# Kernel tuning notes

Measured on AMD Instinct MI355X. Metric: run time of the kernel, lower is better.

The kernel has to match this reference:

```python
import jax, jax.numpy as jnp
from jax import lax
import numpy as np

V, T, K, R, H, EN, L = 10000, 100, 50, 300, 200, 800, 3
B = 128
TRAIN_SIZE = 100000
DELTA = 0.005


def setup_inputs():
    key = jax.random.key(0)
    ks = jax.random.split(key, 16)
    s = 0.02
    return {
        "bows": jax.random.uniform(ks[0], (B, V), jnp.float32) * 10.0 + 1e-3,
        "times": jax.random.randint(ks[1], (B,), 0, T),
        "rnn_inp": jax.random.uniform(ks[2], (T, V), jnp.float32),
        "rho_W": jax.random.normal(ks[3], (V, R), jnp.float32) * s,
        "mu_q_alpha": jax.random.normal(ks[4], (K, T, R), jnp.float32),
        "logsigma_q_alpha": jax.random.normal(ks[5], (K, T, R), jnp.float32) * 0.1 - 2.0,
        "qtheta_W1": jax.random.normal(ks[6], (EN, V + K), jnp.float32) * s,
        "qtheta_b1": jnp.zeros((EN,), jnp.float32),
        "qtheta_W2": jax.random.normal(ks[7], (EN, EN), jnp.float32) * s,
        "qtheta_b2": jnp.zeros((EN,), jnp.float32),
        "mu_theta_W": jax.random.normal(ks[8], (K, EN), jnp.float32) * s,
        "mu_theta_b": jnp.zeros((K,), jnp.float32),
        "ls_theta_W": jax.random.normal(ks[9], (K, EN), jnp.float32) * s,
        "ls_theta_b": jnp.zeros((K,), jnp.float32),
        "eta_map_W": jax.random.normal(ks[10], (H, V), jnp.float32) * s,
        "eta_map_b": jnp.zeros((H,), jnp.float32),
        "lstm_Wih": jax.random.normal(ks[11], (L, 4 * H, H), jnp.float32) * s,
        "lstm_Whh": jax.random.normal(ks[12], (L, 4 * H, H), jnp.float32) * s,
        "lstm_bih": jnp.zeros((L, 4 * H), jnp.float32),
        "lstm_bhh": jnp.zeros((L, 4 * H), jnp.float32),
        "mu_eta_W": jax.random.normal(ks[13], (K, H + K), jnp.float32) * s,
        "mu_eta_b": jnp.zeros((K,), jnp.float32),
        "ls_eta_W": jax.random.normal(ks[14], (K, H + K), jnp.float32) * s,
        "ls_eta_b": jnp.zeros((K,), jnp.float32),
    }


def _kl(q_mu, q_ls, p_mu, p_ls):
    # KL(N(q_mu, exp(q_ls)) || N(p_mu, exp(p_ls))), logsigma == log-variance as in torch code
    return 0.5 * jnp.sum((jnp.exp(q_ls) + (q_mu - p_mu) ** 2) / (jnp.exp(p_ls) + 1e-6) - 1.0 + p_ls - q_ls, axis=-1)


def _lstm(x, Wih, Whh, bih, bhh):
    # x: [T, H]; L stacked LSTM layers (batch of 1 squeezed), torch gate order i,f,g,o
    for l in range(Wih.shape[0]):
        Wi, Wh, bi, bh = Wih[l], Whh[l], bih[l], bhh[l]
        Hd = Wh.shape[1]

        def step(carry, xt, Wi=Wi, Wh=Wh, bi=bi, bh=bh):
            h, c = carry
            g = Wi @ xt + Wh @ h + bi + bh
            i, f, gg, o = jnp.split(g, 4)
            c = jax.nn.sigmoid(f) * c + jax.nn.sigmoid(i) * jnp.tanh(gg)
            h = jax.nn.sigmoid(o) * jnp.tanh(c)
            return (h, c), h

        z = jnp.zeros((Hd,), x.dtype)
        _, x = lax.scan(step, (z, z), x)
    return x


def _forward(bows, rnn_inp, rho_W, mu_q_alpha, logsigma_q_alpha, qtheta_W1, qtheta_b1, qtheta_W2, qtheta_b2, mu_theta_W, mu_theta_b, ls_theta_W, ls_theta_b, eta_map_W, eta_map_b, lstm_Wih, lstm_Whh, lstm_bih, lstm_bhh, mu_eta_W, mu_eta_b, ls_eta_W, ls_eta_b, times):
    log_delta = jnp.log(jnp.float32(DELTA))
    # --- eta: LSTM over word-freq sequence, then sequential mu/logsigma/KL per t ---
    out = _lstm(rnn_inp @ eta_map_W.T + eta_map_b, lstm_Wih, lstm_Whh, lstm_bih, lstm_bhh)  # [T,H]
    p_ls_seq = jnp.concatenate([jnp.zeros((1,), jnp.float32), jnp.full((T - 1,), log_delta, jnp.float32)])

    def eta_step(eta_prev, xs):
        o_t, p_ls = xs
        x = jnp.concatenate([o_t, eta_prev])
        mu = mu_eta_W @ x + mu_eta_b
        ls = ls_eta_W @ x + ls_eta_b
        kl = _kl(mu, ls, eta_prev, jnp.full_like(mu, p_ls))
        return mu, (mu, kl)  # eval-mode reparameterize -> eta_t = mu

    _, (etas, kls) = lax.scan(eta_step, jnp.zeros((K,), jnp.float32), (out, p_ls_seq))
    kl_eta = kls.sum()
    # --- theta encoder ---
    nb = bows / bows.sum(1, keepdims=True)
    eta_td = etas[times]  # [B,K]
    h = jax.nn.relu(jnp.concatenate([nb, eta_td], axis=1) @ qtheta_W1.T + qtheta_b1)
    h = jax.nn.relu(h @ qtheta_W2.T + qtheta_b2)
    mu_t = h @ mu_theta_W.T + mu_theta_b
    ls_t = h @ ls_theta_W.T + ls_theta_b
    theta = jax.nn.softmax(mu_t, axis=-1)  # z = mu (eval-mode reparam)
    coeff = jnp.float32(TRAIN_SIZE / bows.shape[0])
    kl_theta = _kl(mu_t, ls_t, eta_td, jnp.zeros_like(mu_t)).sum() * coeff
    # --- alpha: with eval-mode reparam, alphas == mu, so KL is fully vectorized ---
    muT = jnp.transpose(mu_q_alpha, (1, 0, 2))  # [T,K,R]
    lsT = jnp.transpose(logsigma_q_alpha, (1, 0, 2))
    alphas = muT
    p_mu = jnp.concatenate([jnp.zeros((1, K, R), muT.dtype), alphas[:-1]], axis=0)
    p_ls = jnp.concatenate([jnp.zeros((1, K, R), muT.dtype), jnp.full((T - 1, K, R), log_delta, muT.dtype)], axis=0)
    kl_alpha = _kl(muT, lsT, p_mu, p_ls).sum()
    # --- beta and NLL ---
    logit = alphas.reshape(T * K, R) @ rho_W.T  # [T*K, V]
    beta = jax.nn.softmax(logit, axis=-1).reshape(T, K, V)
    beta_d = beta[times]  # [B,K,V]
    loglik = jnp.log(jnp.einsum('bk,bkv->bv', theta, beta_d) + 1e-12)
    nll = (-(loglik * bows).sum(-1)).sum() * coeff
    loss = nll + kl_eta + kl_theta + kl_alpha
    return loss, nll, kl_eta, kl_theta, kl_alpha


def reference(bows, times, rnn_inp, rho_W, mu_q_alpha, logsigma_q_alpha, qtheta_W1, qtheta_b1, qtheta_W2, qtheta_b2, mu_theta_W, mu_theta_b, ls_theta_W, ls_theta_b, eta_map_W, eta_map_b, lstm_Wih, lstm_Whh, lstm_bih, lstm_bhh, mu_eta_W, mu_eta_b, ls_eta_W, ls_eta_b):
    return _forward(bows, rnn_inp, rho_W, mu_q_alpha, logsigma_q_alpha, qtheta_W1, qtheta_b1, qtheta_W2, qtheta_b2, mu_theta_W, mu_theta_b, ls_theta_W, ls_theta_b, eta_map_W, eta_map_b, lstm_Wih, lstm_Whh, lstm_bih, lstm_bhh, mu_eta_W, mu_eta_b, ls_eta_W, ls_eta_b, times)
```

## Files before the change

kernel.cpp:

```cpp
#include <hip/hip_runtime.h>


typedef unsigned int u32;
typedef unsigned short u16;
typedef _Float16 f16;
typedef f16 f16x2 __attribute__((ext_vector_type(2)));
typedef short bf16x8 __attribute__((ext_vector_type(8)));
typedef float f32x4 __attribute__((ext_vector_type(4)));
typedef u32 u32x4 __attribute__((ext_vector_type(4)));

#define LOG_DELTA (-5.2983174f)
#define COEFF 781.25f

#if defined(__has_builtin)
#if __has_builtin(__builtin_amdgcn_sdot4)
#define HAVE_SDOT4 1
#endif
#endif

__device__ __forceinline__ float bf2f(u16 a) { return __uint_as_float(((u32)a) << 16); }
__device__ __forceinline__ u16 f2bf(float f) {
  u32 u = __float_as_uint(f);
  u32 r = (u + 0x7fffu + ((u >> 16) & 1u)) >> 16;
  return (u16)r;
}
__device__ __forceinline__ int dot4i8(u32 a, u32 b, int c) {
#ifdef HAVE_SDOT4
  return __builtin_amdgcn_sdot4(a, b, c, false);
#else
  int s = c;
  s += ((int)(a << 24) >> 24) * ((int)(b << 24) >> 24);
  s += ((int)(a << 16) >> 24) * ((int)(b << 16) >> 24);
  s += ((int)(a << 8) >> 24) * ((int)(b << 8) >> 24);
  s += ((int)a >> 24) * ((int)b >> 24);
  return s;
#endif
}
__device__ __forceinline__ float sigm(float x) { return 1.f / (1.f + __expf(-x)); }
__device__ __forceinline__ float ftanh(float x) { float t = __expf(2.f * x); return (t - 1.f) / (t + 1.f); }
__device__ __forceinline__ u16 f2h(float x) { return __builtin_bit_cast(u16, (f16)x); }
__device__ __forceinline__ float h2f(u16 x) { return (float)__builtin_bit_cast(f16, x); }
__device__ __forceinline__ void async_load16(const u16* g, u16* l) {
  __builtin_amdgcn_global_load_lds((const __attribute__((address_space(1))) u32*)g,
                                   (__attribute__((address_space(3))) u32*)l, 16, 0, 0);
}

__device__ __forceinline__ void gbar(u32* bar, int idx, u32 target) {
  __syncthreads();
  __threadfence();
  if (threadIdx.x == 0) {
    atomicAdd(&bar[idx], 1u);
    while (atomicAdd(&bar[idx], 0u) < target) __builtin_amdgcn_s_sleep(8);
  }
  __threadfence();
  __syncthreads();
}


__global__ __launch_bounds__(256) void k_init(
    const float* __restrict__ bih, const float* __restrict__ bhh, float* __restrict__ bsum,
    const float* __restrict__ muthb, const float* __restrict__ lsthb, float* __restrict__ mul,
    const float* __restrict__ muq, const float* __restrict__ lsq, float* __restrict__ alphapart,
    float* __restrict__ accum, u32* __restrict__ bar) {
  const int bx = blockIdx.x, tid = threadIdx.x;
  if (bx < 10) {
    int i = bx * 256 + tid;
    if (i < 2400) bsum[i] = bih[i] + bhh[i];
    return;
  }
  if (bx == 10) {
    if (tid < 8) accum[tid] = 0.f;
    else if (tid < 16) bar[tid - 8] = 0u;
    return;
  }
  if (bx < 523) {
    __shared__ float red[256];
    float s = 0.f;
    for (int i = (bx - 11) * 256 + tid; i < 1500000; i += 512 * 256) {
      int r = i % 300;
      int tk = i / 300;
      int k = tk % 50;
      int t = tk / 50;
      size_t idx = (size_t)k * 30000 + (size_t)t * 300 + r;
      float mu = muq[idx], ls = lsq[idx];
      float pm = 0.f, pls = 0.f;
      if (t > 0) { pm = muq[idx - 300]; pls = LOG_DELTA; }
      float d = mu - pm;
      s += 0.5f * ((__expf(ls) + d * d) / (__expf(pls) + 1e-6f) - 1.f + pls - ls);
    }
    red[tid] = s; __syncthreads();
    for (int o = 128; o > 0; o >>= 1) { if (tid < o) red[tid] += red[tid + o]; __syncthreads(); }
    if (tid == 0) alphapart[bx - 11] = red[0];
    return;
  }
  {
    int i = (bx - 523) * 256 + tid;
    if (i < 12800) { int c = i % 100; mul[i] = (c < 50) ? muthb[c] : lsthb[c - 50]; }
  }
}


__global__ __launch_bounds__(256) void k_nbquant(
    const float* __restrict__ bows, float* __restrict__ nb,
    const float* __restrict__ Whh, u32* __restrict__ whq, float* __restrict__ rowscale) {
  const int tid = threadIdx.x;
  if (blockIdx.x < 128) {
    __shared__ float red[256];
    const int b = blockIdx.x;
    float s = 0.f;
    for (int v = tid; v < 10000; v += 256) s += bows[b * 10000 + v];
    red[tid] = s; __syncthreads();
    for (int o = 128; o > 0; o >>= 1) { if (tid < o) red[tid] += red[tid + o]; __syncthreads(); }
    const float inv = 1.f / red[0];
    for (int v = tid; v < 10000; v += 256) nb[b * 10000 + v] = bows[b * 10000 + v] * inv;
    return;
  }
  __shared__ float wrow[4][200];
  const int wave = tid >> 6, lane = tid & 63;
  const int gr = (blockIdx.x - 128) * 4 + wave;
  const float* src = Whh + (size_t)gr * 200;
  float m = 0.f;
  for (int c = lane; c < 200; c += 64) { float v = src[c]; wrow[wave][c] = v; m = fmaxf(m, fabsf(v)); }
  for (int o = 32; o > 0; o >>= 1) m = fmaxf(m, __shfl_down(m, o));
  m = __shfl(m, 0);
  const float qs = (m > 0.f) ? 127.f / m : 0.f;
  const int l = gr / 800, rr = gr - l * 800;
  if (lane < 52) {
    u32 d = 0;
    if (lane < 50) {
#pragma unroll
      for (int b = 0; b < 4; ++b) {
        int q = __float2int_rn(wrow[wave][lane * 4 + b] * qs);
        q = max(-127, min(127, q));
        d |= ((u32)(q & 0xff)) << (8 * b);
      }
    }
    whq[l * 41600 + rr * 52 + lane] = d;
  }
  if (lane == 0) rowscale[gr] = (m > 0.f) ? m / 127.f : 0.f;
}


__global__ __launch_bounds__(256) void k_prepAB(const float* __restrict__ muq,
                                                const float* __restrict__ rho,
                                                u16* __restrict__ Abf, u16* __restrict__ Bbf) {
  if (blockIdx.x < 6400) {
    int idx = blockIdx.x * 256 + threadIdx.x;
    if (idx >= 5120 * 320) return;
    int r = idx % 320, m = idx / 320;
    float v = 0.f;
    if (r < 300 && m < 5000) { int t = m / 50, k = m - t * 50; v = muq[k * 30000 + t * 300 + r]; }
    Abf[idx] = f2bf(v);
    return;
  }
  int idx = (blockIdx.x - 6400) * 256 + threadIdx.x;
  if (idx >= 10112 * 320) return;
  int r = idx % 320, n = idx / 320;
  float v = (r < 300 && n < 10000) ? rho[n * 300 + r] : 0.f;
  Bbf[idx] = f2bf(v);
}


#define ST 64
#define SBK 32

template<int AMODE, int BMODE, int EPI>
__global__ __launch_bounds__(256) void gemm64(
    const float* __restrict__ A, const float* __restrict__ Bm, const float* __restrict__ Bm2,
    const float* __restrict__ bias, float* __restrict__ C,
    int M, int N, int Kd, int lda, int ldb,
    const int* __restrict__ times, const float* __restrict__ etas)
{
  __shared__ __align__(16) float As[SBK][ST + 4];
  __shared__ __align__(16) float Bs[SBK][ST + 4];
  const int tid = threadIdx.x;
  const int tx = tid & 15, ty = tid >> 4;
  const int m_base = blockIdx.x * ST, n_base = blockIdx.y * ST;
  float acc[4][4] = {};
  const int nkt = (Kd + SBK - 1) / SBK;
  const int per = (nkt + gridDim.z - 1) / gridDim.z;
  const int kt0 = blockIdx.z * per;
  const int kt1 = min(nkt, kt0 + per);
  const int lkk = tid & 31;
  const int lrow = tid >> 5;
  for (int kt = kt0; kt < kt1; ++kt) {
    const int kg = kt * SBK + lkk;
#pragma unroll
    for (int i = 0; i < 8; ++i) {
      const int m = m_base + lrow + i * 8;
      float v = 0.f;
      if (m < M && kg < Kd) {
        if (AMODE == 0) v = A[(size_t)m * lda + kg];
        else {
          if (kg < 10000) v = A[(size_t)m * 10000 + kg];
          else v = etas[times[m] * 50 + (kg - 10000)];
        }
      }
      As[lkk][lrow + i * 8] = v;
    }
#pragma unroll
    for (int i = 0; i < 8; ++i) {
      const int n = n_base + lrow + i * 8;
      float v = 0.f;
      if (n < N && kg < Kd) {
        if (BMODE == 0) v = Bm[(size_t)n * ldb + kg];
        else v = (n < 50) ? Bm[(size_t)n * ldb + kg] : Bm2[(size_t)(n - 50) * ldb + kg];
      }
      Bs[lkk][lrow + i * 8] = v;
    }
    __syncthreads();
#pragma unroll
    for (int kk = 0; kk < SBK; ++kk) {
      const float4 a4 = *(const float4*)&As[kk][ty * 4];
      const float4 b4 = *(const float4*)&Bs[kk][tx * 4];
      const float av[4] = {a4.x, a4.y, a4.z, a4.w};
      const float bv[4] = {b4.x, b4.y, b4.z, b4.w};
#pragma unroll
      for (int i = 0; i < 4; ++i)
#pragma unroll
        for (int j = 0; j < 4; ++j) acc[i][j] += av[i] * bv[j];
    }
    __syncthreads();
  }
#pragma unroll
  for (int i = 0; i < 4; ++i) {
    const int m = m_base + ty * 4 + i;
    if (m >= M) continue;
#pragma unroll
    for (int j = 0; j < 4; ++j) {
      const int n = n_base + tx * 4 + j;
      if (n >= N) continue;
      float v = acc[i][j];
      if (EPI == 1) { C[(size_t)m * N + n] = v + bias[n]; }
      else if (EPI == 2) { v += bias[n]; C[(size_t)m * N + n] = v > 0.f ? v : 0.f; }
      else if (EPI == 5) { atomicAdd(&C[(size_t)m * N + n], v); }
      else { C[(size_t)m * N + n] = v; }
    }
  }
}


#define LT 128
#define LBK 32

template<int AMODE>
__global__ __launch_bounds__(256) void gemm128p(
    const float* __restrict__ A, const float* __restrict__ Bm,
    float* __restrict__ P,
    int M, int N, int Kd, int lda, int ldb,
    const int* __restrict__ times, const float* __restrict__ etas)
{
  __shared__ __align__(16) float As[LBK][LT + 4];
  __shared__ __align__(16) float Bs[LBK][LT + 4];
  const int tid = threadIdx.x;
  const int tx = tid & 15, ty = tid >> 4;
  const int m_base = blockIdx.x * LT, n_base = blockIdx.y * LT;
  const int nkt = (Kd + LBK - 1) / LBK;
  const int per = (nkt + gridDim.z - 1) / gridDim.z;
  const int kt0 = blockIdx.z * per;
  const int kt1 = min(nkt, kt0 + per);
  const int lkk = tid & 31;
  const int lrow = tid >> 5;
  float acc[8][8] = {};
  float pa[16], pb[16];
  {
    const int kg = kt0 * LBK + lkk;
#pragma unroll
    for (int i = 0; i < 16; ++i) {
      const int m = m_base + lrow + i * 8;
      float v = 0.f;
      if (m < M && kg < Kd) {
        if (AMODE == 0) v = A[(size_t)m * lda + kg];
        else v = (kg < 10000) ? A[(size_t)m * 10000 + kg] : etas[times[m] * 50 + (kg - 10000)];
      }
      pa[i] = v;
      const int n = n_base + lrow + i * 8;
      float w = 0.f;
      if (n < N && kg < Kd) w = Bm[(size_t)n * ldb + kg];
      pb[i] = w;
    }
  }
  for (int kt = kt0; kt < kt1; ++kt) {
#pragma unroll
    for (int i = 0; i < 16; ++i) {
      As[lkk][lrow + i * 8] = pa[i];
      Bs[lkk][lrow + i * 8] = pb[i];
    }
    __syncthreads();
    if (kt + 1 < kt1) {
      const int kg = (kt + 1) * LBK + lkk;
#pragma unroll
      for (int i = 0; i < 16; ++i) {
        const int m = m_base + lrow + i * 8;
        float v = 0.f;
        if (m < M && kg < Kd) {
          if (AMODE == 0) v = A[(size_t)m * lda + kg];
          else v = (kg < 10000) ? A[(size_t)m * 10000 + kg] : etas[times[m] * 50 + (kg - 10000)];
        }
        pa[i] = v;
        const int n = n_base + lrow + i * 8;
        float w = 0.f;
        if (n < N && kg < Kd) w = Bm[(size_t)n * ldb + kg];
        pb[i] = w;
      }
    }
#pragma unroll
    for (int kk = 0; kk < LBK; ++kk) {
      const float4* ap = (const float4*)&As[kk][ty * 8];
      const float4* bp = (const float4*)&Bs[kk][tx * 8];
      const float4 a0 = ap[0], a1 = ap[1];
      const float4 b0 = bp[0], b1 = bp[1];
      const float av[8] = {a0.x, a0.y, a0.z, a0.w, a1.x, a1.y, a1.z, a1.w};
      const float bv[8] = {b0.x, b0.y, b0.z, b0.w, b1.x, b1.y, b1.z, b1.w};
#pragma unroll
      for (int i = 0; i < 8; ++i)
#pragma unroll
        for (int j = 0; j < 8; ++j) acc[i][j] += av[i] * bv[j];
    }
    __syncthreads();
  }
  float* Cz = P + (size_t)blockIdx.z * M * N;
#pragma unroll
  for (int i = 0; i < 8; ++i) {
    const int m = m_base + ty * 8 + i;
    if (m >= M) continue;
#pragma unroll
    for (int j = 0; j < 8; ++j) {
      const int n = n_base + tx * 8 + j;
      if (n >= N) continue;
      Cz[(size_t)m * N + n] = acc[i][j];
    }
  }
}

template<int EPI>
__global__ __launch_bounds__(256) void k_reduceZ(const float* __restrict__ P,
                                                 const float* __restrict__ bias,
                                                 float* __restrict__ out,
                                                 int N, int total, int Z) {
  for (int i = blockIdx.x * 256 + threadIdx.x; i < total; i += gridDim.x * 256) {
    float s = bias[i % N];
    for (int z = 0; z < Z; ++z) s += P[(size_t)z * total + i];
    if (EPI == 2) s = s > 0.f ? s : 0.f;
    out[i] = s;
  }
}


__global__ __launch_bounds__(256) void gemm_mfma_bT(
    const u16* __restrict__ A, const u16* __restrict__ B, u16* __restrict__ C,
    int M, int N)
{
  __shared__ u16 As[128 * 32];
  __shared__ u16 Bs[128 * 32];
  const int tid = threadIdx.x;
  const int l = tid & 63, w = tid >> 6;
  const int wm = w & 1, wn = w >> 1;
  const int m0 = blockIdx.x * 128, n0 = blockIdx.y * 128;
  f32x4 acc[4][4] = {};
  const int arow = l >> 2;
  const int acol = (l & 3) * 8;
  for (int kt = 0; kt < 10; ++kt) {
    const int k0 = kt * 32;
#pragma unroll
    for (int c = 0; c < 2; ++c) {
      const int i = w + c * 4;
      async_load16(A + (size_t)(m0 + i * 16 + arow) * 320 + k0 + acol, As + i * 512);
      async_load16(B + (size_t)(n0 + i * 16 + arow) * 320 + k0 + acol, Bs + i * 512);
    }
    __syncthreads();
    bf16x8 af[4], bfr[4];
#pragma unroll
    for (int x = 0; x < 4; ++x) {
      af[x]  = *(const bf16x8*)&As[(wm * 64 + x * 16 + (l & 15)) * 32 + (l >> 4) * 8];
      bfr[x] = *(const bf16x8*)&Bs[(wn * 64 + x * 16 + (l & 15)) * 32 + (l >> 4) * 8];
    }
#pragma unroll
    for (int x = 0; x < 4; ++x)
#pragma unroll
      for (int y = 0; y < 4; ++y)
        acc[x][y] = __builtin_amdgcn_mfma_f32_16x16x32_bf16(af[x], bfr[y], acc[x][y], 0, 0, 0);
    __syncthreads();
  }
  const int col = l & 15, quad = l >> 4;
#pragma unroll
  for (int x = 0; x < 4; ++x) {
    const int gmB = m0 + wm * 64 + x * 16 + quad * 4;
#pragma unroll
    for (int y = 0; y < 4; ++y) {
      const int gn = n0 + wn * 64 + y * 16 + col;
      if (gn >= N) continue;
#pragma unroll
      for (int r = 0; r < 4; ++r) {
        const int gm = gmB + r;
        if (gm < M) C[(size_t)gm * N + gn] = f2bf(acc[x][y][r]);
      }
    }
  }
}


#define NBLK 27

__device__ void mv800(const float* __restrict__ W, const float* __restrict__ lin,
                      const float* __restrict__ bias, float* __restrict__ outp, int bi) {
  const int gw = bi * 8 + (threadIdx.x >> 6);
  const int lane = threadIdx.x & 63;
  for (int r = gw; r < 800; r += NBLK * 8) {
    const float* Wr = W + (size_t)r * 200;
    const float bv = bias[r];
    for (int tt = lane; tt < 100; tt += 64) {
      const float* xr = lin + tt * 200;
      float a0 = 0.f, a1 = 0.f, a2 = 0.f, a3 = 0.f;
#pragma unroll 10
      for (int k = 0; k < 200; k += 4) {
        a0 += Wr[k] * xr[k];     a1 += Wr[k + 1] * xr[k + 1];
        a2 += Wr[k + 2] * xr[k + 2]; a3 += Wr[k + 3] * xr[k + 3];
      }
      outp[tt * 800 + r] = (a0 + a1) + (a2 + a3) + bv;
    }
  }
}

__device__ void mv_pc0(const float* __restrict__ muW, const float* __restrict__ lsW,
                       const float* __restrict__ mub, const float* __restrict__ lsb,
                       const float* __restrict__ hsC, float* __restrict__ pc0, int bi) {
  const int gw = bi * 8 + (threadIdx.x >> 6);
  const int lane = threadIdx.x & 63;
  for (int j = gw; j < 100; j += NBLK * 8) {
    const float* Wr = (j < 50) ? (muW + (size_t)j * 250) : (lsW + (size_t)(j - 50) * 250);
    const float bv = (j < 50) ? mub[j] : lsb[j - 50];
    for (int tt = lane; tt < 100; tt += 64) {
      const float* xr = hsC + tt * 200;
      float a0 = 0.f, a1 = 0.f, a2 = 0.f, a3 = 0.f;
#pragma unroll 10
      for (int k = 0; k < 200; k += 4) {
        a0 += Wr[k] * xr[k];     a1 += Wr[k + 1] * xr[k + 1];
        a2 += Wr[k + 2] * xr[k + 2]; a3 += Wr[k + 3] * xr[k + 3];
      }
      pc0[tt * 100 + j] = (a0 + a1) + (a2 + a3) + bv;
    }
  }
}

__device__ void scan_body(const u32* __restrict__ whq, const float* __restrict__ rowscale,
                          const float* __restrict__ xproj, float* __restrict__ hseq) {
  __shared__ u16 pg[800];
  __shared__ __align__(16) u32 hq[52];
  __shared__ float wmax[8];
  __shared__ float hscale_s[1];
  const int tid = threadIdx.x;
  const int act = (tid < 400);
  const int rA = act ? tid : 399;
  const u32x4* gA = (const u32x4*)(whq + (size_t)rA * 52);
  const u32x4* gB = (const u32x4*)(whq + (size_t)(rA + 400) * 52);
  u32x4 wA4[13], wB4[13];
#pragma unroll
  for (int i = 0; i < 13; ++i) { wA4[i] = gA[i]; wB4[i] = gB[i]; }
  float rsA = 0.f, rsB = 0.f, xpA = 0.f, xpB = 0.f;
  if (act) {
    rsA = rowscale[tid]; rsB = rowscale[tid + 400];
    xpA = xproj[tid]; xpB = xproj[tid + 400];
  }
  if (tid < 52) hq[tid] = 0;
  if (tid < 8) wmax[tid] = 0.f;
  if (tid == 0) hscale_s[0] = 0.f;
  float c_reg = 0.f;
  __syncthreads();
  for (int t = 0; t < 100; ++t) {
    if (act) {
      float nxA = 0.f, nxB = 0.f;
      if (t < 99) { nxA = xproj[(t + 1) * 800 + tid]; nxB = xproj[(t + 1) * 800 + tid + 400]; }
      const float hdq = hscale_s[0];
      u32x4 hv4[13];
#pragma unroll
      for (int i = 0; i < 13; ++i) hv4[i] = *((const u32x4*)hq + i);
      int aA = 0, aB = 0;
#pragma unroll
      for (int g = 0; g < 50; ++g) {
        const u32 h = hv4[g >> 2][g & 3];
        aA = dot4i8(wA4[g >> 2][g & 3], h, aA);
        aB = dot4i8(wB4[g >> 2][g & 3], h, aB);
      }
      pg[tid] = f2h((float)aA * (rsA * hdq) + xpA);
      pg[tid + 400] = f2h((float)aB * (rsB * hdq) + xpB);
      xpA = nxA; xpB = nxB;
    }
    __syncthreads();
    float hv = 0.f;
    if (tid < 200) {
      float gi = sigm(h2f(pg[tid]));
      float gf = sigm(h2f(pg[200 + tid]));
      float gg = ftanh(h2f(pg[400 + tid]));
      float go = sigm(h2f(pg[600 + tid]));
      c_reg = gf * c_reg + gi * gg;
      hv = go * ftanh(c_reg);
      hseq[t * 200 + tid] = hv;
    }
    float m = fabsf(hv);
    for (int o = 32; o > 0; o >>= 1) m = fmaxf(m, __shfl_down(m, o));
    if ((tid & 63) == 0) wmax[tid >> 6] = m;
    __syncthreads();
    if (tid < 200) {
      const float hm = fmaxf(fmaxf(wmax[0], wmax[1]), fmaxf(wmax[2], wmax[3]));
      const float qs = (hm > 0.f) ? 127.f / hm : 0.f;
      int q = __float2int_rn(hv * qs);
      q = max(-127, min(127, q));
      ((signed char*)hq)[tid] = (signed char)q;
      if (tid == 0) hscale_s[0] = (hm > 0.f) ? hm / 127.f : 0.f;
    }
    __syncthreads();
  }
}

__device__ void eta_body(const float* __restrict__ muW, const float* __restrict__ lsW,
                         const float* __restrict__ pc0, float* __restrict__ etas,
                         float* __restrict__ accum) {
  __shared__ __align__(16) float ep[52];
  const int j = threadIdx.x;
  const int act = (j < 50);
  const int jc = act ? j : 49;
  const float* bm = muW + (size_t)jc * 250 + 200;
  const float* bl = lsW + (size_t)jc * 250 + 200;
  float wmu[52], wls[52];
#pragma unroll
  for (int k = 0; k < 25; ++k) {
    float2 a = *(const float2*)(bm + 2 * k);
    float2 b = *(const float2*)(bl + 2 * k);
    wmu[2 * k] = a.x; wmu[2 * k + 1] = a.y;
    wls[2 * k] = b.x; wls[2 * k + 1] = b.y;
  }
  wmu[50] = wmu[51] = wls[50] = wls[51] = 0.f;
  if (j < 52) ep[j] = 0.f;
  float klacc = 0.f;
  float mye = 0.f;
  float pmu = act ? pc0[j] : 0.f;
  float pls_ = act ? pc0[50 + j] : 0.f;
  __syncthreads();
  for (int t = 0; t < 100; ++t) {
    float nmu = 0.f, nls = 0.f;
    if (act && t < 99) { nmu = pc0[(t + 1) * 100 + j]; nls = pc0[(t + 1) * 100 + 50 + j]; }
    float ma[4] = {pmu, 0.f, 0.f, 0.f};
    float la[4] = {pls_, 0.f, 0.f, 0.f};
    const float4* e4 = (const float4*)ep;
#pragma unroll
    for (int i = 0; i < 13; ++i) {
      const float4 e = e4[i];
      ma[0] += wmu[4 * i + 0] * e.x; ma[1] += wmu[4 * i + 1] * e.y;
      ma[2] += wmu[4 * i + 2] * e.z; ma[3] += wmu[4 * i + 3] * e.w;
      la[0] += wls[4 * i + 0] * e.x; la[1] += wls[4 * i + 1] * e.y;
      la[2] += wls[4 * i + 2] * e.z; la[3] += wls[4 * i + 3] * e.w;
    }
    const float mu = (ma[0] + ma[1]) + (ma[2] + ma[3]);
    const float ls = (la[0] + la[1]) + (la[2] + la[3]);
    __syncthreads();
    if (act) {
      const float pls = (t == 0) ? 0.f : LOG_DELTA;
      const float pv = __expf(pls) + 1e-6f;
      const float d = mu - mye;
      klacc += 0.5f * ((__expf(ls) + d * d) / pv - 1.f + pls - ls);
      etas[t * 50 + j] = mu;
      mye = mu;
      ep[j] = mu;
    }
    __syncthreads();
    pmu = nmu; pls_ = nls;
  }
  for (int o = 32; o > 0; o >>= 1) klacc += __shfl_down(klacc, o);
  if (j == 0) accum[0] = klacc;
}

__global__ __launch_bounds__(512, 1) void lstm_chain(
    const u32* __restrict__ whq, const float* __restrict__ rowsc,
    const float* __restrict__ Wih, const float* __restrict__ bsum,
    const float* __restrict__ x0, float* __restrict__ xproj,
    float* __restrict__ hsA, float* __restrict__ hsB, float* __restrict__ hsC,
    const float* __restrict__ mueW, const float* __restrict__ lseW,
    const float* __restrict__ mueb, const float* __restrict__ lseb,
    float* __restrict__ pc0, float* __restrict__ etas, float* __restrict__ accum,
    u32* __restrict__ bar)
{
  const int bi = blockIdx.x;
  const float* lin[3] = {x0, hsA, hsB};
  float* lout[3] = {hsA, hsB, hsC};
  for (int l = 0; l < 3; ++l) {
    mv800(Wih + (size_t)l * 160000, lin[l], bsum + l * 800, xproj, bi);
    gbar(bar, 2 * l, NBLK);
    if (bi == 0) scan_body(whq + (size_t)l * 41600, rowsc + l * 800, xproj, lout[l]);
    gbar(bar, 2 * l + 1, NBLK);
  }
  mv_pc0(mueW, lseW, mueb, lseb, hsC, pc0, bi);
  gbar(bar, 6, NBLK);
  if (bi == 0) eta_body(mueW, lseW, pc0, etas, accum);
}


__global__ __launch_bounds__(64) void k_theta(const float* __restrict__ mul,
                                              const float* __restrict__ etas, const int* __restrict__ times,
                                              float* __restrict__ theta, float* __restrict__ accum) {
  const int b = blockIdx.x, lane = threadIdx.x;
  float m_ = 0.f, l_ = 0.f, e_ = 0.f, mx = -1e30f;
  if (lane < 50) {
    m_ = mul[b * 100 + lane];
    l_ = mul[b * 100 + 50 + lane];
    e_ = etas[times[b] * 50 + lane];
    mx = m_;
  }
  for (int o = 32; o > 0; o >>= 1) mx = fmaxf(mx, __shfl_down(mx, o));
  mx = __shfl(mx, 0);
  float ex = (lane < 50) ? __expf(m_ - mx) : 0.f;
  float sum = ex;
  for (int o = 32; o > 0; o >>= 1) sum += __shfl_down(sum, o);
  sum = __shfl(sum, 0);
  if (lane < 50) theta[b * 50 + lane] = ex / sum;
  float kl = 0.f;
  if (lane < 50) {
    float d = m_ - e_;
    kl = 0.5f * ((__expf(l_) + d * d) / (1.f + 1e-6f) - 1.f - l_);
  }
  for (int o = 32; o > 0; o >>= 1) kl += __shfl_down(kl, o);
  if (lane == 0) atomicAdd(accum + 1, kl);
}


__global__ __launch_bounds__(256) void k_rowsum(const u16* __restrict__ logit, float* __restrict__ Z) {
  const int r = blockIdx.x, tid = threadIdx.x;
  const u32* row = (const u32*)(logit + (size_t)r * 10000);
  __shared__ float red[256];
  float s = 0.f;
  for (int v = tid; v < 5000; v += 256) {
    u32 p = row[v];
    s += __expf(bf2f((u16)(p & 0xffffu))) + __expf(bf2f((u16)(p >> 16)));
  }
  red[tid] = s; __syncthreads();
  for (int o = 128; o > 0; o >>= 1) { if (tid < o) red[tid] += red[tid + o]; __syncthreads(); }
  if (tid == 0) Z[r] = red[0];
}


__global__ __launch_bounds__(256) void k_nll(const u16* __restrict__ logit, const float* __restrict__ Z,
                                             const float* __restrict__ theta, const float* __restrict__ bows,
                                             const int* __restrict__ times, float* __restrict__ accum) {
  const int b = blockIdx.x, seg = blockIdx.y, tid = threadIdx.x;
  const int t = times[b];
  __shared__ float c2[52];
  __shared__ float red[256];
  if (tid < 50) c2[tid] = theta[b * 50 + tid] / Z[t * 50 + tid];
  __syncthreads();
  float part = 0.f;
  const int v0 = seg * 1250, v1 = v0 + 1250;
  const u16* base = logit + (size_t)t * 500000;
  for (int v = v0 + tid; v < v1; v += 256) {
    float ssv = 1e-12f;
#pragma unroll
    for (int k = 0; k < 50; ++k) ssv += c2[k] * __expf(bf2f(base[k * 10000 + v]));
    part += bows[b * 10000 + v] * __logf(ssv);
  }
  red[tid] = part; __syncthreads();
  for (int o = 128; o > 0; o >>= 1) { if (tid < o) red[tid] += red[tid + o]; __syncthreads(); }
  if (tid == 0) atomicAdd(accum + 3, -red[0]);
}


__global__ __launch_bounds__(64) void k_final(const float* __restrict__ accum,
                                              const float* __restrict__ alphapart,
                                              float* __restrict__ out) {
  const int tid = threadIdx.x;
  float s = 0.f;
  for (int i = tid; i < 512; i += 64) s += alphapart[i];
  for (int o = 32; o > 0; o >>= 1) s += __shfl_down(s, o);
  if (tid == 0) {
    float nll = accum[3] * COEFF;
    float kl_eta = accum[0];
    float kl_theta = accum[1] * COEFF;
    float kl_alpha = s;
    out[0] = nll + kl_eta + kl_theta + kl_alpha;
    out[1] = nll;
    out[2] = kl_eta;
    out[3] = kl_theta;
    out[4] = kl_alpha;
  }
}


extern "C" void kernel_launch(void* const* d_in, const int* in_sizes, int n_in,
                              void* d_out, int out_size, void* d_ws, size_t ws_size,
                              hipStream_t stream) {
  (void)in_sizes; (void)n_in; (void)out_size; (void)ws_size;
  const float* bows   = (const float*)d_in[0];
  const int*   times  = (const int*)d_in[1];
  const float* rnn_in = (const float*)d_in[2];
  const float* rho_W  = (const float*)d_in[3];
  const float* muq    = (const float*)d_in[4];
  const float* lsq    = (const float*)d_in[5];
  const float* qW1    = (const float*)d_in[6];
  const float* qb1    = (const float*)d_in[7];
  const float* qW2    = (const float*)d_in[8];
  const float* qb2    = (const float*)d_in[9];
  const float* muthW  = (const float*)d_in[10];
  const float* muthb  = (const float*)d_in[11];
  const float* lsthW  = (const float*)d_in[12];
  const float* lsthb  = (const float*)d_in[13];
  const float* emW    = (const float*)d_in[14];
  const float* emb    = (const float*)d_in[15];
  const float* Wih    = (const float*)d_in[16];
  const float* Whh    = (const float*)d_in[17];
  const float* bih    = (const float*)d_in[18];
  const float* bhh    = (const float*)d_in[19];
  const float* mueW   = (const float*)d_in[20];
  const float* mueb   = (const float*)d_in[21];
  const float* lseW   = (const float*)d_in[22];
  const float* lseb   = (const float*)d_in[23];
  float* out = (float*)d_out;
  float* ws = (float*)d_ws;

  float* accum = ws + 0;
  float* nb    = ws + 8;
  float* x0    = ws + 1280008;
  float* xproj = ws + 1300008;
  float* hsA   = ws + 1380008;
  float* hsB   = ws + 1400008;
  u32*   whq   = (u32*)(ws + 1420008);
  float* rowsc = ws + 1544808;
  u32*   bar   = (u32*)(ws + 1547208);
  float* pc0   = ws + 1547408;
  float* alphp = ws + 1558008;
  float* hsC   = ws + 1560008;
  float* bsum  = ws + 1660008;
  float* etas  = ws + 1662408;
  float* h1    = ws + 1667408;
  float* h2    = ws + 1769808;
  float* mul   = ws + 1872208;
  float* theta = ws + 1885008;
  float* Zrow  = ws + 1891408;
  u16*   A_bf  = (u16*)(ws + 1896408);
  u16*   B_bf  = (u16*)(ws + 2715608);
  u16*   logit = (u16*)(ws + 4333528);
  float* P1    = ws + 4333528;
  float* Px0   = ws + 8941528;
  float* P2    = ws + 10221528;

  k_init<<<573, 256, 0, stream>>>(bih, bhh, bsum, muthb, lsthb, mul,
                                  muq, lsq, alphp, accum, bar);
  k_nbquant<<<728, 256, 0, stream>>>(bows, nb, Whh, whq, rowsc);
  k_prepAB<<<19040, 256, 0, stream>>>(muq, rho_W, A_bf, B_bf);

  gemm128p<0><<<dim3(1, 2, 64), 256, 0, stream>>>(rnn_in, emW, Px0,
                                                  100, 200, 10000, 10000, 10000, nullptr, nullptr);
  k_reduceZ<1><<<79, 256, 0, stream>>>(Px0, emb, x0, 200, 20000, 64);

  lstm_chain<<<NBLK, 512, 0, stream>>>(whq, rowsc, Wih, bsum, x0, xproj,
                                       hsA, hsB, hsC, mueW, lseW, mueb, lseb,
                                       pc0, etas, accum, bar);

  gemm128p<2><<<dim3(1, 7, 45), 256, 0, stream>>>(nb, qW1, P1,
                                                  128, 800, 10050, 10000, 10050, times, etas);
  k_reduceZ<2><<<400, 256, 0, stream>>>(P1, qb1, h1, 800, 102400, 45);
  gemm128p<0><<<dim3(1, 7, 5), 256, 0, stream>>>(h1, qW2, P2,
                                                 128, 800, 800, 800, 800, nullptr, nullptr);
  k_reduceZ<2><<<400, 256, 0, stream>>>(P2, qb2, h2, 800, 102400, 5);
  gemm64<0, 1, 5><<<dim3(2, 2, 5), 256, 0, stream>>>(h2, muthW, lsthW, nullptr, mul,
                                                     128, 100, 800, 800, 800, nullptr, nullptr);
  k_theta<<<128, 64, 0, stream>>>(mul, etas, times, theta, accum);

  gemm_mfma_bT<<<dim3(40, 79), 256, 0, stream>>>(A_bf, B_bf, logit, 5000, 10000);
  k_rowsum<<<5000, 256, 0, stream>>>(logit, Zrow);
  k_nll<<<dim3(128, 8), 256, 0, stream>>>(logit, Zrow, theta, bows, times, accum);

  k_final<<<1, 64, 0, stream>>>(accum, alphp, out);
}
```

Measured before the change: 1.294 ms.

## Replace persistent LSTM chain with separate GEMM and scan kernel launches

The single persistent lstm_chain kernel, which used software grid barriers across 27 blocks and scalar matrix-vector loops for the input projections, is split into separate launches. Each layer now runs a tiled gemm64 for the input projection followed by a single-block scan kernel, and the eta projection likewise uses gemm64 plus its own scan kernel. This removes the spin-wait barriers and the naive per-row dot products, at the cost of eight extra kernel launches on the serial critical path. The eta biases are packed into a new buffer in k_init so the gemm epilogue can add them.

```diff
diff --git a/kernel.cpp b/kernel.cpp
--- a/kernel.cpp
+++ b/kernel.cpp
@@ -45,23 +45,13 @@
                                    (__attribute__((address_space(3))) u32*)l, 16, 0, 0);
 }
 
-__device__ __forceinline__ void gbar(u32* bar, int idx, u32 target) {
-  __syncthreads();
-  __threadfence();
-  if (threadIdx.x == 0) {
-    atomicAdd(&bar[idx], 1u);
-    while (atomicAdd(&bar[idx], 0u) < target) __builtin_amdgcn_s_sleep(8);
-  }
-  __threadfence();
-  __syncthreads();
-}
-
 
 __global__ __launch_bounds__(256) void k_init(
     const float* __restrict__ bih, const float* __restrict__ bhh, float* __restrict__ bsum,
     const float* __restrict__ muthb, const float* __restrict__ lsthb, float* __restrict__ mul,
     const float* __restrict__ muq, const float* __restrict__ lsq, float* __restrict__ alphapart,
-    float* __restrict__ accum, u32* __restrict__ bar) {
+    const float* __restrict__ mueb, const float* __restrict__ lseb, float* __restrict__ bias2e,
+    float* __restrict__ accum) {
   const int bx = blockIdx.x, tid = threadIdx.x;
   if (bx < 10) {
     int i = bx * 256 + tid;
@@ -70,7 +60,6 @@
   }
   if (bx == 10) {
     if (tid < 8) accum[tid] = 0.f;
-    else if (tid < 16) bar[tid - 8] = 0u;
     return;
   }
   if (bx < 523) {
@@ -93,9 +82,13 @@
     if (tid == 0) alphapart[bx - 11] = red[0];
     return;
   }
-  {
+  if (bx < 573) {
     int i = (bx - 523) * 256 + tid;
     if (i < 12800) { int c = i % 100; mul[i] = (c < 50) ? muthb[c] : lsthb[c - 50]; }
+    return;
+  }
+  {
+    if (tid < 100) bias2e[tid] = (tid < 50) ? mueb[tid] : lseb[tid - 50];
   }
 }
 
@@ -400,51 +393,12 @@
 }
 
 
-#define NBLK 27
-
-__device__ void mv800(const float* __restrict__ W, const float* __restrict__ lin,
-                      const float* __restrict__ bias, float* __restrict__ outp, int bi) {
-  const int gw = bi * 8 + (threadIdx.x >> 6);
-  const int lane = threadIdx.x & 63;
-  for (int r = gw; r < 800; r += NBLK * 8) {
-    const float* Wr = W + (size_t)r * 200;
-    const float bv = bias[r];
-    for (int tt = lane; tt < 100; tt += 64) {
-      const float* xr = lin + tt * 200;
-      float a0 = 0.f, a1 = 0.f, a2 = 0.f, a3 = 0.f;
-#pragma unroll 10
-      for (int k = 0; k < 200; k += 4) {
-        a0 += Wr[k] * xr[k];     a1 += Wr[k + 1] * xr[k + 1];
-        a2 += Wr[k + 2] * xr[k + 2]; a3 += Wr[k + 3] * xr[k + 3];
-      }
-      outp[tt * 800 + r] = (a0 + a1) + (a2 + a3) + bv;
-    }
-  }
-}
-
-__device__ void mv_pc0(const float* __restrict__ muW, const float* __restrict__ lsW,
-                       const float* __restrict__ mub, const float* __restrict__ lsb,
-                       const float* __restrict__ hsC, float* __restrict__ pc0, int bi) {
-  const int gw = bi * 8 + (threadIdx.x >> 6);
-  const int lane = threadIdx.x & 63;
-  for (int j = gw; j < 100; j += NBLK * 8) {
-    const float* Wr = (j < 50) ? (muW + (size_t)j * 250) : (lsW + (size_t)(j - 50) * 250);
-    const float bv = (j < 50) ? mub[j] : lsb[j - 50];
-    for (int tt = lane; tt < 100; tt += 64) {
-      const float* xr = hsC + tt * 200;
-      float a0 = 0.f, a1 = 0.f, a2 = 0.f, a3 = 0.f;
-#pragma unroll 10
-      for (int k = 0; k < 200; k += 4) {
-        a0 += Wr[k] * xr[k];     a1 += Wr[k + 1] * xr[k + 1];
-        a2 += Wr[k + 2] * xr[k + 2]; a3 += Wr[k + 3] * xr[k + 3];
-      }
-      pc0[tt * 100 + j] = (a0 + a1) + (a2 + a3) + bv;
-    }
-  }
-}
-
-__device__ void scan_body(const u32* __restrict__ whq, const float* __restrict__ rowscale,
-                          const float* __restrict__ xproj, float* __restrict__ hseq) {
+__global__ __launch_bounds__(512, 1) void lstm_scan_reg(
+    const u32* __restrict__ whq,
+    const float* __restrict__ rowscale,
+    const float* __restrict__ xproj,
+    float* __restrict__ hseq)
+{
   __shared__ u16 pg[800];
   __shared__ __align__(16) u32 hq[52];
   __shared__ float wmax[8];
@@ -513,24 +467,29 @@
   }
 }
 
-__device__ void eta_body(const float* __restrict__ muW, const float* __restrict__ lsW,
-                         const float* __restrict__ pc0, float* __restrict__ etas,
-                         float* __restrict__ accum) {
+
+__global__ __launch_bounds__(64, 1) void eta_scan_reg(
+    const float* __restrict__ muW, const float* __restrict__ lsW,
+    const float* __restrict__ pc0,
+    float* __restrict__ etas, float* __restrict__ accum)
+{
   __shared__ __align__(16) float ep[52];
   const int j = threadIdx.x;
   const int act = (j < 50);
-  const int jc = act ? j : 49;
-  const float* bm = muW + (size_t)jc * 250 + 200;
-  const float* bl = lsW + (size_t)jc * 250 + 200;
   float wmu[52], wls[52];
-#pragma unroll
-  for (int k = 0; k < 25; ++k) {
-    float2 a = *(const float2*)(bm + 2 * k);
-    float2 b = *(const float2*)(bl + 2 * k);
-    wmu[2 * k] = a.x; wmu[2 * k + 1] = a.y;
-    wls[2 * k] = b.x; wls[2 * k + 1] = b.y;
-  }
-  wmu[50] = wmu[51] = wls[50] = wls[51] = 0.f;
+  if (act) {
+#pragma unroll
+    for (int k = 0; k < 25; ++k) {
+      float2 a = *(const float2*)(muW + (size_t)j * 250 + 200 + 2 * k);
+      float2 b = *(const float2*)(lsW + (size_t)j * 250 + 200 + 2 * k);
+      wmu[2 * k] = a.x; wmu[2 * k + 1] = a.y;
+      wls[2 * k] = b.x; wls[2 * k + 1] = b.y;
+    }
+    wmu[50] = wmu[51] = wls[50] = wls[51] = 0.f;
+  } else {
+#pragma unroll
+    for (int k = 0; k < 52; ++k) { wmu[k] = 0.f; wls[k] = 0.f; }
+  }
   if (j < 52) ep[j] = 0.f;
   float klacc = 0.f;
   float mye = 0.f;
@@ -568,30 +527,6 @@
   }
   for (int o = 32; o > 0; o >>= 1) klacc += __shfl_down(klacc, o);
   if (j == 0) accum[0] = klacc;
-}
-
-__global__ __launch_bounds__(512, 1) void lstm_chain(
-    const u32* __restrict__ whq, const float* __restrict__ rowsc,
-    const float* __restrict__ Wih, const float* __restrict__ bsum,
-    const float* __restrict__ x0, float* __restrict__ xproj,
-    float* __restrict__ hsA, float* __restrict__ hsB, float* __restrict__ hsC,
-    const float* __restrict__ mueW, const float* __restrict__ lseW,
-    const float* __restrict__ mueb, const float* __restrict__ lseb,
-    float* __restrict__ pc0, float* __restrict__ etas, float* __restrict__ accum,
-    u32* __restrict__ bar)
-{
-  const int bi = blockIdx.x;
-  const float* lin[3] = {x0, hsA, hsB};
-  float* lout[3] = {hsA, hsB, hsC};
-  for (int l = 0; l < 3; ++l) {
-    mv800(Wih + (size_t)l * 160000, lin[l], bsum + l * 800, xproj, bi);
-    gbar(bar, 2 * l, NBLK);
-    if (bi == 0) scan_body(whq + (size_t)l * 41600, rowsc + l * 800, xproj, lout[l]);
-    gbar(bar, 2 * l + 1, NBLK);
-  }
-  mv_pc0(mueW, lseW, mueb, lseb, hsC, pc0, bi);
-  gbar(bar, 6, NBLK);
-  if (bi == 0) eta_body(mueW, lseW, pc0, etas, accum);
 }
 
 
@@ -722,7 +657,7 @@
   float* hsB   = ws + 1400008;
   u32*   whq   = (u32*)(ws + 1420008);
   float* rowsc = ws + 1544808;
-  u32*   bar   = (u32*)(ws + 1547208);
+  float* bias2e= ws + 1547208;
   float* pc0   = ws + 1547408;
   float* alphp = ws + 1558008;
   float* hsC   = ws + 1560008;
@@ -740,8 +675,8 @@
   float* Px0   = ws + 8941528;
   float* P2    = ws + 10221528;
 
-  k_init<<<573, 256, 0, stream>>>(bih, bhh, bsum, muthb, lsthb, mul,
-                                  muq, lsq, alphp, accum, bar);
+  k_init<<<574, 256, 0, stream>>>(bih, bhh, bsum, muthb, lsthb, mul,
+                                  muq, lsq, alphp, mueb, lseb, bias2e, accum);
   k_nbquant<<<728, 256, 0, stream>>>(bows, nb, Whh, whq, rowsc);
   k_prepAB<<<19040, 256, 0, stream>>>(muq, rho_W, A_bf, B_bf);
 
@@ -749,9 +684,17 @@
                                                   100, 200, 10000, 10000, 10000, nullptr, nullptr);
   k_reduceZ<1><<<79, 256, 0, stream>>>(Px0, emb, x0, 200, 20000, 64);
 
-  lstm_chain<<<NBLK, 512, 0, stream>>>(whq, rowsc, Wih, bsum, x0, xproj,
-                                       hsA, hsB, hsC, mueW, lseW, mueb, lseb,
-                                       pc0, etas, accum, bar);
+  const float* lin[3] = {x0, hsA, hsB};
+  float* lout[3] = {hsA, hsB, hsC};
+  for (int l = 0; l < 3; ++l) {
+    gemm64<0, 0, 1><<<dim3(2, 13, 1), 256, 0, stream>>>(lin[l], Wih + l * 160000, nullptr,
+                                                        bsum + l * 800, xproj,
+                                                        100, 800, 200, 200, 200, nullptr, nullptr);
+    lstm_scan_reg<<<1, 512, 0, stream>>>(whq + l * 41600, rowsc + l * 800, xproj, lout[l]);
+  }
+  gemm64<0, 1, 1><<<dim3(2, 2, 1), 256, 0, stream>>>(hsC, mueW, lseW, bias2e, pc0,
+                                                     100, 100, 200, 200, 250, nullptr, nullptr);
+  eta_scan_reg<<<1, 64, 0, stream>>>(mueW, lseW, pc0, etas, accum);
 
   gemm128p<2><<<dim3(1, 7, 45), 256, 0, stream>>>(nb, qW1, P1,
                                                   128, 800, 10050, 10000, 10050, times, etas);
```

After: 1.127 ms. -12.9%, faster.
